# Performance work log

Measured on AMD Instinct MI355X. Metric: run time of the kernel, lower is better.

The kernel has to match this reference:

```python
import jax, jax.numpy as jnp
import numpy as np

B, K, D = 32768, 4096, 256


def setup_inputs() -> dict:
    key = jax.random.key(0)
    k1, k2 = jax.random.split(key)
    z_e_x = jax.random.normal(k1, (B, D), dtype=jnp.float32)
    # embedding.weight initialized N(0, 1) per init='normal'
    weight = jax.random.normal(k2, (K, D), dtype=jnp.float32)
    return {"z_e_x": z_e_x, "weight": weight}


def reference(z_e_x, weight):
    # Squared L2 distances ||z - e||^2 = ||z||^2 - 2 z.e + ||e||^2,
    # computed via a GEMM instead of materializing the [B, K, D] broadcast
    # that the torch code builds with repeat(). Same math as
    # sum((z_e_x_ - codebook_vectors)**2, dim=-1).
    z_sq = jnp.sum(z_e_x * z_e_x, axis=-1, keepdims=True)          # [B, 1]
    e_sq = jnp.sum(weight * weight, axis=-1)                        # [K]
    cross = jnp.einsum('bd,kd->bk', z_e_x, weight)                  # [B, K]
    distances = z_sq - 2.0 * cross + e_sq                           # [B, K]
    # greedy=True path of forward()
    index = jnp.argmin(distances, axis=-1)                          # [B] int
    # straight_through(): quantized lookup + straight-through estimator
    z_q_x = weight[index]                                           # [B, D]
    sg_z_e_x = z_e_x + jax.lax.stop_gradient(z_q_x - z_e_x)         # [B, D]
    return (sg_z_e_x, z_q_x, index)
```

## Files before the change

kernel.cpp:

```cpp
#include <hip/hip_runtime.h>

typedef _Float16 half8 __attribute__((ext_vector_type(8)));
typedef _Float16 half4 __attribute__((ext_vector_type(4)));
typedef float floatx16 __attribute__((ext_vector_type(16)));

constexpr int Bn = 32768, Kn = 4096, Dn = 256;
constexpr int BM = 128;
constexpr int BNS = 64;
constexpr int NI = Kn / BNS;
constexpr int NCH = NI * 4;

__global__ void prep_kernel(const float* __restrict__ w, float* __restrict__ esq,
                            char* __restrict__ w16) {
    int code = blockIdx.x * 4 + (threadIdx.x >> 6);
    int l = threadIdx.x & 63;
    float4 v = *reinterpret_cast<const float4*>(w + (size_t)code * Dn + l * 4);
    float s = v.x * v.x + v.y * v.y + v.z * v.z + v.w * v.w;
    #pragma unroll
    for (int off = 32; off; off >>= 1) s += __shfl_xor(s, off);
    if (l == 0) esq[code] = s;

    float fv[4] = {v.x, v.y, v.z, v.w};
    half4 h, lo;
    #pragma unroll
    for (int j = 0; j < 4; ++j) {
        _Float16 hh = (_Float16)fv[j];
        h[j] = hh;
        lo[j] = (_Float16)(fv[j] - (float)hh);
    }
    const int kc = l >> 4;
    const int o_h = (l & 15) * 8;
    const int swz = (code & 15) << 4;
    char* row = w16 + (size_t)code * 1024 + kc * 256;
    *reinterpret_cast<half4*>(row + (o_h ^ swz)) = h;
    *reinterpret_cast<half4*>(row + ((o_h + 128) ^ swz)) = lo;
}

#define GLDS(gsrc, ldsoff)                                                        \
    __builtin_amdgcn_global_load_lds(                                             \
        (const __attribute__((address_space(1))) unsigned int*)(const void*)(gsrc),\
        (__attribute__((address_space(3))) unsigned int*)(void*)(smem + (ldsoff)), \
        16, 0, 0)

#define MFMA(a, b, c) __builtin_amdgcn_mfma_f32_32x32x16_f16((a), (b), (c), 0, 0, 0)

__launch_bounds__(256, 1)
__global__ void vq_kernel(const float* __restrict__ z, const float* __restrict__ w,
                          const float* __restrict__ esq, const char* __restrict__ w16,
                          float* __restrict__ out0, float* __restrict__ out1,
                          float* __restrict__ out2) {
    __shared__ char smem[84480];
    const int tid = threadIdx.x;
    const int wv = tid >> 6, l = tid & 63;
    const int mw = wv >> 1, nw = wv & 1;
    const int lh = l >> 5, ll = l & 31;
    const int blkRow = blockIdx.x * BM;

    float* esq_s = reinterpret_cast<float*>(smem + 65536);
    #pragma unroll
    for (int j = 0; j < 16; ++j) esq_s[j * 256 + tid] = esq[j * 256 + tid];

    half8 a_hi[2][16], a_lo[2][16];
    #pragma unroll
    for (int t = 0; t < 2; ++t) {
        const float* zr = z + (size_t)(blkRow + mw * 64 + t * 32 + ll) * Dn + lh * 8;
        #pragma unroll
        for (int ks = 0; ks < 16; ++ks) {
            float4 f0 = *reinterpret_cast<const float4*>(zr + ks * 16);
            float4 f1 = *reinterpret_cast<const float4*>(zr + ks * 16 + 4);
            float fv[8] = {f0.x, f0.y, f0.z, f0.w, f1.x, f1.y, f1.z, f1.w};
            #pragma unroll
            for (int j = 0; j < 8; ++j) {
                _Float16 h = (_Float16)fv[j];
                a_hi[t][ks][j] = h;
                a_lo[t][ks][j] = (_Float16)(fv[j] - (float)h);
            }
        }
    }

    const int G0 = wv * 256 + l;
    const size_t srcOff0 = (size_t)(G0 >> 4) * 1024 + (G0 & 15) * 16;

    int addrH[4], addrL[4];
    {
        const int c_loc = nw * 32 + ll;
        const int swz = (c_loc & 15) << 4;
        #pragma unroll
        for (int ks = 0; ks < 4; ++ks) {
            const int o = ks * 32 + lh * 16;
            addrH[ks] = c_loc * 256 + (o ^ swz);
            addrL[ks] = c_loc * 256 + ((o + 128) ^ swz);
        }
    }

    float rbv0[16], rbv1[16];
    int rbi0[16], rbi1[16];
    #pragma unroll
    for (int q = 0; q < 16; ++q) { rbv0[q] = 3.4e38f; rbv1[q] = 3.4e38f; rbi0[q] = 0; rbi1[q] = 0; }

    asm volatile("s_waitcnt vmcnt(0)" ::: "memory");
    __syncthreads();

    {
        const char* s0 = w16 + srcOff0;
        const char* s1 = w16 + 256 + srcOff0;
        const int d0 = wv * 4096, d1 = 16384 + wv * 4096;
        GLDS(s0, d0); GLDS(s0 + 4096, d0 + 1024); GLDS(s0 + 8192, d0 + 2048); GLDS(s0 + 12288, d0 + 3072);
        GLDS(s1, d1); GLDS(s1 + 4096, d1 + 1024); GLDS(s1 + 8192, d1 + 2048); GLDS(s1 + 12288, d1 + 3072);
    }

    for (int ni = 0; ni < NI; ++ni) {
        floatx16 acc0 = {}, acc1 = {};
        #pragma unroll
        for (int kc = 0; kc < 4; ++kc) {
            const int c = ni * 4 + kc;
            if (c + 2 < NCH) {
                const char* s2 = w16 + (size_t)((c + 2) >> 2) * 65536 + ((c + 2) & 3) * 256 + srcOff0;
                const int d2 = (((kc + 2) & 3) * 16384) + wv * 4096;
                GLDS(s2, d2); GLDS(s2 + 4096, d2 + 1024);
                GLDS(s2 + 8192, d2 + 2048); GLDS(s2 + 12288, d2 + 3072);
                asm volatile("s_waitcnt vmcnt(8)" ::: "memory");
            } else if (c + 1 < NCH) {
                asm volatile("s_waitcnt vmcnt(4)" ::: "memory");
            } else {
                asm volatile("s_waitcnt vmcnt(0)" ::: "memory");
            }
            __builtin_amdgcn_s_barrier();
            asm volatile("" ::: "memory");
            const char* base = smem + kc * 16384;
            __builtin_amdgcn_s_setprio(1);
            #pragma unroll
            for (int ks = 0; ks < 4; ++ks) {
                const half8 bh = *reinterpret_cast<const half8*>(base + addrH[ks]);
                const half8 bl = *reinterpret_cast<const half8*>(base + addrL[ks]);
                const int ksg = kc * 4 + ks;
                acc0 = MFMA(a_hi[0][ksg], bh, acc0);
                acc1 = MFMA(a_hi[1][ksg], bh, acc1);
                acc0 = MFMA(a_hi[0][ksg], bl, acc0);
                acc1 = MFMA(a_hi[1][ksg], bl, acc1);
                acc0 = MFMA(a_lo[0][ksg], bh, acc0);
                acc1 = MFMA(a_lo[1][ksg], bh, acc1);
            }
            __builtin_amdgcn_s_setprio(0);
        }
        const float e = esq_s[ni * 64 + nw * 32 + ll];
        const int col = ni * 64 + nw * 32 + ll;
        #pragma unroll
        for (int q = 0; q < 16; ++q) {
            const float v0 = fmaf(-2.f, acc0[q], e);
            if (v0 < rbv0[q]) { rbv0[q] = v0; rbi0[q] = col; }
            const float v1 = fmaf(-2.f, acc1[q], e);
            if (v1 < rbv1[q]) { rbv1[q] = v1; rbi1[q] = col; }
        }
    }

    #pragma unroll
    for (int off = 1; off < 32; off <<= 1) {
        #pragma unroll
        for (int q = 0; q < 16; ++q) {
            float ov0 = __shfl_xor(rbv0[q], off); int oi0 = __shfl_xor(rbi0[q], off);
            if (ov0 < rbv0[q] || (ov0 == rbv0[q] && oi0 < rbi0[q])) { rbv0[q] = ov0; rbi0[q] = oi0; }
            float ov1 = __shfl_xor(rbv1[q], off); int oi1 = __shfl_xor(rbi1[q], off);
            if (ov1 < rbv1[q] || (ov1 == rbv1[q] && oi1 < rbi1[q])) { rbv1[q] = ov1; rbi1[q] = oi1; }
        }
    }

    __syncthreads();
    int2* comb = reinterpret_cast<int2*>(smem + 81920);
    if (ll == 0) {
        #pragma unroll
        for (int q = 0; q < 16; ++q) {
            const int r32 = (q & 3) + 8 * (q >> 2) + 4 * lh;
            comb[(mw * 64 + r32) * 2 + nw] = make_int2(__float_as_int(rbv0[q]), rbi0[q]);
            comb[(mw * 64 + 32 + r32) * 2 + nw] = make_int2(__float_as_int(rbv1[q]), rbi1[q]);
        }
    }
    __syncthreads();
    int* idxF = reinterpret_cast<int*>(smem + 83968);
    if (tid < 128) {
        int2 c0 = comb[tid * 2], c1 = comb[tid * 2 + 1];
        float v0 = __int_as_float(c0.x), v1 = __int_as_float(c1.x);
        idxF[tid] = (v1 < v0 || (v1 == v0 && c1.y < c0.y)) ? c1.y : c0.y;
    }
    __syncthreads();

    {
        const int r = tid >> 1, p2 = tid & 1;
        const int gRow = blkRow + r;
        const int idx = idxF[r];
        const float* wr = w + (size_t)idx * Dn + p2 * 128;
        const float* zr = z + (size_t)gRow * Dn + p2 * 128;
        float* o0 = out0 + (size_t)gRow * Dn + p2 * 128;
        float* o1 = out1 + (size_t)gRow * Dn + p2 * 128;
        #pragma unroll
        for (int q = 0; q < 32; ++q) {
            float4 wq = *reinterpret_cast<const float4*>(wr + q * 4);
            float4 zq = *reinterpret_cast<const float4*>(zr + q * 4);
            *reinterpret_cast<float4*>(o1 + q * 4) = wq;
            float4 sg;
            sg.x = zq.x + (wq.x - zq.x);
            sg.y = zq.y + (wq.y - zq.y);
            sg.z = zq.z + (wq.z - zq.z);
            sg.w = zq.w + (wq.w - zq.w);
            *reinterpret_cast<float4*>(o0 + q * 4) = sg;
        }
        if (p2 == 0) out2[gRow] = (float)idx;
    }
}

extern "C" void kernel_launch(void* const* d_in, const int* in_sizes, int n_in,
                              void* d_out, int out_size, void* d_ws, size_t ws_size,
                              hipStream_t stream) {
    (void)in_sizes; (void)n_in; (void)out_size; (void)ws_size;
    const float* z = (const float*)d_in[0];
    const float* w = (const float*)d_in[1];
    float* esq = (float*)d_ws;
    char* w16 = (char*)d_ws + 16384;
    float* out0 = (float*)d_out;
    float* out1 = out0 + (size_t)Bn * Dn;
    float* out2 = out1 + (size_t)Bn * Dn;

    prep_kernel<<<Kn / 4, 256, 0, stream>>>(w, esq, w16);
    vq_kernel<<<Bn / BM, 256, 0, stream>>>(z, w, esq, w16, out0, out1, out2);
}
```

Measured before the change: 319.0 us.

## Register double-buffer B fragments and pack argmin indices into bytes

B fragments for the next K-chunk are now read from LDS into a second register set while the MFMAs run on the current set, so LDS read latency overlaps with matrix math. The running argmin indices are stored as 8-bit tile numbers packed four per register, which frees VGPRs for the extra fragment buffers. The final cross-lane reduction loops per q to keep fewer values live, and waves_per_eu(1,1) is pinned. The prefetch wait drops from vmcnt(8) to vmcnt(4), which may add stalls on global-to-LDS loads, and higher register pressure could cause spills.

```diff
diff --git a/kernel.cpp b/kernel.cpp
--- a/kernel.cpp
+++ b/kernel.cpp
@@ -6,9 +6,8 @@
 
 constexpr int Bn = 32768, Kn = 4096, Dn = 256;
 constexpr int BM = 128;
-constexpr int BNS = 64;
-constexpr int NI = Kn / BNS;
-constexpr int NCH = NI * 4;
+constexpr int NI = 64;
+constexpr int NCH = 256;
 
 __global__ void prep_kernel(const float* __restrict__ w, float* __restrict__ esq,
                             char* __restrict__ w16) {
@@ -44,11 +43,13 @@
 
 #define MFMA(a, b, c) __builtin_amdgcn_mfma_f32_32x32x16_f16((a), (b), (c), 0, 0, 0)
 
+__global__ void
 __launch_bounds__(256, 1)
-__global__ void vq_kernel(const float* __restrict__ z, const float* __restrict__ w,
-                          const float* __restrict__ esq, const char* __restrict__ w16,
-                          float* __restrict__ out0, float* __restrict__ out1,
-                          float* __restrict__ out2) {
+__attribute__((amdgpu_waves_per_eu(1, 1)))
+vq_kernel(const float* __restrict__ z, const float* __restrict__ w,
+          const float* __restrict__ esq, const char* __restrict__ w16,
+          float* __restrict__ out0, float* __restrict__ out1,
+          float* __restrict__ out2) {
     __shared__ char smem[84480];
     const int tid = threadIdx.x;
     const int wv = tid >> 6, l = tid & 63;
@@ -60,7 +61,7 @@
     #pragma unroll
     for (int j = 0; j < 16; ++j) esq_s[j * 256 + tid] = esq[j * 256 + tid];
 
-    half8 a_hi[2][16], a_lo[2][16];
+    half8 a_hi[32], a_lo[32];
     #pragma unroll
     for (int t = 0; t < 2; ++t) {
         const float* zr = z + (size_t)(blkRow + mw * 64 + t * 32 + ll) * Dn + lh * 8;
@@ -72,8 +73,8 @@
             #pragma unroll
             for (int j = 0; j < 8; ++j) {
                 _Float16 h = (_Float16)fv[j];
-                a_hi[t][ks][j] = h;
-                a_lo[t][ks][j] = (_Float16)(fv[j] - (float)h);
+                a_hi[t * 16 + ks][j] = h;
+                a_lo[t * 16 + ks][j] = (_Float16)(fv[j] - (float)h);
             }
         }
     }
@@ -94,9 +95,9 @@
     }
 
     float rbv0[16], rbv1[16];
-    int rbi0[16], rbi1[16];
-    #pragma unroll
-    for (int q = 0; q < 16; ++q) { rbv0[q] = 3.4e38f; rbv1[q] = 3.4e38f; rbi0[q] = 0; rbi1[q] = 0; }
+    unsigned rbn0[4] = {0, 0, 0, 0}, rbn1[4] = {0, 0, 0, 0};
+    #pragma unroll
+    for (int q = 0; q < 16; ++q) { rbv0[q] = 3.4e38f; rbv1[q] = 3.4e38f; }
 
     asm volatile("s_waitcnt vmcnt(0)" ::: "memory");
     __syncthreads();
@@ -107,6 +108,16 @@
         const int d0 = wv * 4096, d1 = 16384 + wv * 4096;
         GLDS(s0, d0); GLDS(s0 + 4096, d0 + 1024); GLDS(s0 + 8192, d0 + 2048); GLDS(s0 + 12288, d0 + 3072);
         GLDS(s1, d1); GLDS(s1 + 4096, d1 + 1024); GLDS(s1 + 8192, d1 + 2048); GLDS(s1 + 12288, d1 + 3072);
+    }
+    asm volatile("s_waitcnt vmcnt(4)" ::: "memory");
+    __builtin_amdgcn_s_barrier();
+    asm volatile("" ::: "memory");
+
+    half8 sh0[4], sl0[4], sh1[4], sl1[4];
+    #pragma unroll
+    for (int ks = 0; ks < 4; ++ks) {
+        sh0[ks] = *reinterpret_cast<const half8*>(smem + addrH[ks]);
+        sl0[ks] = *reinterpret_cast<const half8*>(smem + addrL[ks]);
     }
 
     for (int ni = 0; ni < NI; ++ni) {
@@ -119,60 +130,85 @@
                 const int d2 = (((kc + 2) & 3) * 16384) + wv * 4096;
                 GLDS(s2, d2); GLDS(s2 + 4096, d2 + 1024);
                 GLDS(s2 + 8192, d2 + 2048); GLDS(s2 + 12288, d2 + 3072);
-                asm volatile("s_waitcnt vmcnt(8)" ::: "memory");
-            } else if (c + 1 < NCH) {
                 asm volatile("s_waitcnt vmcnt(4)" ::: "memory");
             } else {
                 asm volatile("s_waitcnt vmcnt(0)" ::: "memory");
             }
             __builtin_amdgcn_s_barrier();
             asm volatile("" ::: "memory");
-            const char* base = smem + kc * 16384;
-            __builtin_amdgcn_s_setprio(1);
-            #pragma unroll
-            for (int ks = 0; ks < 4; ++ks) {
-                const half8 bh = *reinterpret_cast<const half8*>(base + addrH[ks]);
-                const half8 bl = *reinterpret_cast<const half8*>(base + addrL[ks]);
-                const int ksg = kc * 4 + ks;
-                acc0 = MFMA(a_hi[0][ksg], bh, acc0);
-                acc1 = MFMA(a_hi[1][ksg], bh, acc1);
-                acc0 = MFMA(a_hi[0][ksg], bl, acc0);
-                acc1 = MFMA(a_hi[1][ksg], bl, acc1);
-                acc0 = MFMA(a_lo[0][ksg], bh, acc0);
-                acc1 = MFMA(a_lo[1][ksg], bh, acc1);
+            const char* nb = smem + ((kc + 1) & 3) * 16384;
+            if (kc & 1) {
+                if (c + 1 < NCH) {
+                    #pragma unroll
+                    for (int ks = 0; ks < 4; ++ks) {
+                        sh0[ks] = *reinterpret_cast<const half8*>(nb + addrH[ks]);
+                        sl0[ks] = *reinterpret_cast<const half8*>(nb + addrL[ks]);
+                    }
+                }
+                __builtin_amdgcn_s_setprio(1);
+                #pragma unroll
+                for (int ks = 0; ks < 4; ++ks) {
+                    const int ksg = kc * 4 + ks;
+                    acc0 = MFMA(a_hi[ksg], sh1[ks], acc0);
+                    acc1 = MFMA(a_hi[16 + ksg], sh1[ks], acc1);
+                    acc0 = MFMA(a_hi[ksg], sl1[ks], acc0);
+                    acc1 = MFMA(a_hi[16 + ksg], sl1[ks], acc1);
+                    acc0 = MFMA(a_lo[ksg], sh1[ks], acc0);
+                    acc1 = MFMA(a_lo[16 + ksg], sh1[ks], acc1);
+                }
+                __builtin_amdgcn_s_setprio(0);
+            } else {
+                if (c + 1 < NCH) {
+                    #pragma unroll
+                    for (int ks = 0; ks < 4; ++ks) {
+                        sh1[ks] = *reinterpret_cast<const half8*>(nb + addrH[ks]);
+                        sl1[ks] = *reinterpret_cast<const half8*>(nb + addrL[ks]);
+                    }
+                }
+                __builtin_amdgcn_s_setprio(1);
+                #pragma unroll
+                for (int ks = 0; ks < 4; ++ks) {
+                    const int ksg = kc * 4 + ks;
+                    acc0 = MFMA(a_hi[ksg], sh0[ks], acc0);
+                    acc1 = MFMA(a_hi[16 + ksg], sh0[ks], acc1);
+                    acc0 = MFMA(a_hi[ksg], sl0[ks], acc0);
+                    acc1 = MFMA(a_hi[16 + ksg], sl0[ks], acc1);
+                    acc0 = MFMA(a_lo[ksg], sh0[ks], acc0);
+                    acc1 = MFMA(a_lo[16 + ksg], sh0[ks], acc1);
+                }
+                __builtin_amdgcn_s_setprio(0);
             }
-            __builtin_amdgcn_s_setprio(0);
         }
         const float e = esq_s[ni * 64 + nw * 32 + ll];
-        const int col = ni * 64 + nw * 32 + ll;
         #pragma unroll
         for (int q = 0; q < 16; ++q) {
+            const int sh = (q & 3) * 8;
+            const unsigned msk = ~(255u << sh);
             const float v0 = fmaf(-2.f, acc0[q], e);
-            if (v0 < rbv0[q]) { rbv0[q] = v0; rbi0[q] = col; }
+            if (v0 < rbv0[q]) { rbv0[q] = v0; rbn0[q >> 2] = (rbn0[q >> 2] & msk) | ((unsigned)ni << sh); }
             const float v1 = fmaf(-2.f, acc1[q], e);
-            if (v1 < rbv1[q]) { rbv1[q] = v1; rbi1[q] = col; }
-        }
-    }
-
-    #pragma unroll
-    for (int off = 1; off < 32; off <<= 1) {
-        #pragma unroll
-        for (int q = 0; q < 16; ++q) {
-            float ov0 = __shfl_xor(rbv0[q], off); int oi0 = __shfl_xor(rbi0[q], off);
-            if (ov0 < rbv0[q] || (ov0 == rbv0[q] && oi0 < rbi0[q])) { rbv0[q] = ov0; rbi0[q] = oi0; }
-            float ov1 = __shfl_xor(rbv1[q], off); int oi1 = __shfl_xor(rbi1[q], off);
-            if (ov1 < rbv1[q] || (ov1 == rbv1[q] && oi1 < rbi1[q])) { rbv1[q] = ov1; rbi1[q] = oi1; }
+            if (v1 < rbv1[q]) { rbv1[q] = v1; rbn1[q >> 2] = (rbn1[q >> 2] & msk) | ((unsigned)ni << sh); }
         }
     }
 
     __syncthreads();
     int2* comb = reinterpret_cast<int2*>(smem + 81920);
-    if (ll == 0) {
-        #pragma unroll
-        for (int q = 0; q < 16; ++q) {
+    #pragma unroll
+    for (int q = 0; q < 16; ++q) {
+        float v0 = rbv0[q], v1 = rbv1[q];
+        int i0 = (int)((rbn0[q >> 2] >> ((q & 3) * 8)) & 255u) * 64 + nw * 32 + ll;
+        int i1 = (int)((rbn1[q >> 2] >> ((q & 3) * 8)) & 255u) * 64 + nw * 32 + ll;
+        #pragma unroll
+        for (int off = 1; off < 32; off <<= 1) {
+            float ov0 = __shfl_xor(v0, off); int oi0 = __shfl_xor(i0, off);
+            if (ov0 < v0 || (ov0 == v0 && oi0 < i0)) { v0 = ov0; i0 = oi0; }
+            float ov1 = __shfl_xor(v1, off); int oi1 = __shfl_xor(i1, off);
+            if (ov1 < v1 || (ov1 == v1 && oi1 < i1)) { v1 = ov1; i1 = oi1; }
+        }
+        if (ll == 0) {
             const int r32 = (q & 3) + 8 * (q >> 2) + 4 * lh;
-            comb[(mw * 64 + r32) * 2 + nw] = make_int2(__float_as_int(rbv0[q]), rbi0[q]);
-            comb[(mw * 64 + 32 + r32) * 2 + nw] = make_int2(__float_as_int(rbv1[q]), rbi1[q]);
+            comb[(mw * 64 + r32) * 2 + nw] = make_int2(__float_as_int(v0), i0);
+            comb[(mw * 64 + 32 + r32) * 2 + nw] = make_int2(__float_as_int(v1), i1);
         }
     }
     __syncthreads();
```

Result: no change. 318.7 us (-0.1%).
